# Kernel tuning notes

Hardware: AMD Instinct MI355X
Metric: run time of the kernel (lower is better)

Reference implementation:

```python
import jax, jax.numpy as jnp
import numpy as np

B, H, S, DH = 2, 16, 2048, 64

def setup_inputs() -> dict:
    key = jax.random.key(0)
    k1, k2, k3 = jax.random.split(key, 3)
    return {
        "query": jax.random.normal(k1, (B, H, S, DH), dtype=jnp.float32),
        "key": jax.random.normal(k2, (B, H, S, DH), dtype=jnp.float32),
        "value": jax.random.normal(k3, (B, H, S, DH), dtype=jnp.float32),
        "key_padding_mask": jnp.zeros((B, S), dtype=bool),
    }

def reference(query, key, value, key_padding_mask):
    # scores: [B, H, Sq, Sk]
    scale = 1.0 / jnp.sqrt(jnp.asarray(query.shape[-1], query.dtype))
    scores = jnp.einsum("bhqd,bhkd->bhqk", query, key) * scale
    # key padding mask broadcasts over heads and query positions
    scores = jnp.where(key_padding_mask[:, None, None, :], -jnp.inf, scores)
    attn = jax.nn.softmax(scores, axis=-1)
    # dropout is identity in eval mode (deterministic reference)
    out = jnp.einsum("bhqk,bhkd->bhqd", attn, value)
    # [B, H, S, Dh] -> [B, S, H*Dh]
    b, h, s, dh = out.shape
    return out.transpose(0, 2, 1, 3).reshape(b, s, h * dh)
```

## Files before the change

### kernel.cpp

```cpp
#include <hip/hip_runtime.h>

typedef __attribute__((ext_vector_type(4))) float f32x4;
typedef __attribute__((ext_vector_type(4))) short s16x4;
typedef __attribute__((ext_vector_type(8))) short s16x8;

constexpr int Bn = 2, Hn = 16, Sn = 2048, DHn = 64;
constexpr int TQ = 64;
constexpr int TK = 64;
constexpr int NT = Sn / TK;
constexpr int TILE_SH = TK * DHn;
constexpr float SHIFT = 16.0f;

__device__ __forceinline__ unsigned pk2(float a, float b) {
  unsigned ua = __builtin_bit_cast(unsigned, a);
  unsigned ub = __builtin_bit_cast(unsigned, b);
  ua += 0x7fffu + ((ua >> 16) & 1u);
  ub += 0x7fffu + ((ub >> 16) & 1u);
  return (ua >> 16) | (ub & 0xffff0000u);
}

__device__ __forceinline__ float fexp2(float x) {
#if __has_builtin(__builtin_amdgcn_exp2f)
  return __builtin_amdgcn_exp2f(x);
#else
  return exp2f(x);
#endif
}

__device__ __forceinline__ void gl2lds16(const short* g, short* l) {
  __builtin_amdgcn_global_load_lds(
      (const __attribute__((address_space(1))) void*)g,
      (__attribute__((address_space(3))) void*)l, 16, 0, 0);
}

__global__ __launch_bounds__(256, 4)
void prepack_kernel(const float* __restrict__ Kg, const float* __restrict__ Vg,
                    const unsigned char* __restrict__ maskg,
                    short* __restrict__ Kp, short* __restrict__ Vp,
                    float* __restrict__ biasg) {
  const int blk = blockIdx.x;
  const int tid = threadIdx.x;
  const float* Kt = Kg + (size_t)blk * TILE_SH;
  const float* Vt = Vg + (size_t)blk * TILE_SH;
  short* Kd = Kp + (size_t)blk * TILE_SH;
  short* Vd = Vp + (size_t)blk * TILE_SH;

  {
    const int r = tid >> 2;
    const int cb = (tid & 3) * 2;
#pragma unroll
    for (int cc = 0; cc < 2; ++cc) {
      int c = cb + cc;
      const float4* p = (const float4*)(Kt + (size_t)r * DHn + c * 8);
      float4 x = p[0], y = p[1];
      union { unsigned u[4]; s16x8 v; } tmp;
      tmp.u[0] = pk2(x.x, x.y); tmp.u[1] = pk2(x.z, x.w);
      tmp.u[2] = pk2(y.x, y.y); tmp.u[3] = pk2(y.z, y.w);
      *(s16x8*)&Kd[r * 64 + (c ^ (r & 7)) * 8] = tmp.v;
    }
  }
  {
    const int d = tid & 63;
    const int kb = (tid >> 6) * 16;
#pragma unroll
    for (int cc = 0; cc < 2; ++cc) {
      int k0 = kb + cc * 8;
      float v0[8];
#pragma unroll
      for (int j = 0; j < 8; ++j) v0[j] = Vt[(size_t)(k0 + j) * DHn + d];
      union { unsigned u[4]; s16x8 v; } tmp;
      tmp.u[0] = pk2(v0[0], v0[1]); tmp.u[1] = pk2(v0[2], v0[3]);
      tmp.u[2] = pk2(v0[4], v0[5]); tmp.u[3] = pk2(v0[6], v0[7]);
      int c = k0 >> 3;
      *(s16x8*)&Vd[d * 64 + (c ^ (d & 7)) * 8] = tmp.v;
    }
  }
  if (tid < TK) {
    const int bh = blk >> 5, t = blk & 31, b = bh >> 4;
    biasg[b * Sn + t * TK + tid] = maskg[b * Sn + t * TK + tid] ? -1e30f : -SHIFT;
  }
}

__global__ __launch_bounds__(128, 2)
void fattn_kernel(const float* __restrict__ Qg, const short* __restrict__ Kp,
                  const short* __restrict__ Vp, const float* __restrict__ biasg,
                  float* __restrict__ Og) {
  __shared__ __align__(16) short Ksh[2][TILE_SH];
  __shared__ __align__(16) short VTsh[2][TILE_SH];
  __shared__ __align__(16) short Psh[2 * 32 * 64];

  const int tid  = threadIdx.x;
  const int w    = tid >> 6;
  const int lane = tid & 63;
  const int n    = lane & 15;
  const int q4   = lane >> 4;
  const int swz  = n & 7;

  const int blk = blockIdx.x;
  const int bh  = blk & 31;
  const int qt  = blk >> 5;
  const int b   = bh >> 4;
  const int h   = bh & 15;

  const float* Qb = Qg + (size_t)bh * Sn * DHn;
  const short* Kt0 = Kp + (size_t)bh * NT * TILE_SH;
  const short* Vt0 = Vp + (size_t)bh * NT * TILE_SH;
  const float* bq0 = biasg + (size_t)b * Sn;

  const int q0 = qt * TQ + w * 32;

#pragma unroll
  for (int k = 0; k < 4; ++k) {
    gl2lds16(Kt0 + k * 1024 + tid * 8, &Ksh[0][k * 1024 + w * 512]);
    gl2lds16(Vt0 + k * 1024 + tid * 8, &VTsh[0][k * 1024 + w * 512]);
  }

  const float c1 = 0.125f * 1.4426950408889634f;
  s16x8 qf[2][2];
#pragma unroll
  for (int qg = 0; qg < 2; ++qg) {
    const float* qrow = Qb + (size_t)(q0 + qg * 16 + n) * DHn;
#pragma unroll
    for (int kc = 0; kc < 2; ++kc) {
      const float4* p = (const float4*)(qrow + kc * 32 + q4 * 8);
      float4 x = p[0], y = p[1];
      union { unsigned u[4]; s16x8 v; } tmp;
      tmp.u[0] = pk2(x.x * c1, x.y * c1);
      tmp.u[1] = pk2(x.z * c1, x.w * c1);
      tmp.u[2] = pk2(y.x * c1, y.y * c1);
      tmp.u[3] = pk2(y.z * c1, y.w * c1);
      qf[qg][kc] = tmp.v;
    }
  }

  const int c0    = q4 ^ swz;
  const int offA  = n * 64 + c0 * 8;
  const int offB  = n * 64 + (c0 ^ 4) * 8;
  const int prowA = (w * 32 + n) * 64;
  const int pc    = (q4 >> 1) ^ swz;
  const int pwo   = (q4 & 1) * 4;

  f32x4 Oa[2][4];
#pragma unroll
  for (int qg = 0; qg < 2; ++qg)
#pragma unroll
    for (int na = 0; na < 4; ++na) Oa[qg][na] = (f32x4){0.f, 0.f, 0.f, 0.f};
  float lsum[2] = {0.f, 0.f};

  for (int t = 0; t < NT; ++t) {
    const int cur = t & 1;
    __syncthreads();

    f32x4 bias[4];
    {
      const float* bq = bq0 + t * TK + q4 * 4;
#pragma unroll
      for (int mc = 0; mc < 4; ++mc) bias[mc] = *(const f32x4*)(bq + mc * 16);
    }
    asm volatile("" ::: "memory");

    if (t + 1 < NT) {
      const short* Ka = Kt0 + (t + 1) * TILE_SH;
      const short* Va = Vt0 + (t + 1) * TILE_SH;
#pragma unroll
      for (int k = 0; k < 4; ++k) {
        gl2lds16(Ka + k * 1024 + tid * 8, &Ksh[1 - cur][k * 1024 + w * 512]);
        gl2lds16(Va + k * 1024 + tid * 8, &VTsh[1 - cur][k * 1024 + w * 512]);
      }
    }

    s16x8 kf[4][2];
#pragma unroll
    for (int mc = 0; mc < 4; ++mc) {
      kf[mc][0] = *(const s16x8*)&Ksh[cur][mc * 1024 + offA];
      kf[mc][1] = *(const s16x8*)&Ksh[cur][mc * 1024 + offB];
    }

#pragma unroll
    for (int qg = 0; qg < 2; ++qg) {
      f32x4 sa[4];
#pragma unroll
      for (int mc = 0; mc < 4; ++mc) sa[mc] = bias[mc];
#pragma unroll
      for (int mc = 0; mc < 4; ++mc)
#pragma unroll
        for (int kc = 0; kc < 2; ++kc)
          sa[mc] = __builtin_amdgcn_mfma_f32_16x16x32_bf16(kf[mc][kc], qf[qg][kc], sa[mc], 0, 0, 0);

      const int prow = prowA + qg * (16 * 64);
      float ls = 0.f;
#pragma unroll
      for (int mc = 0; mc < 4; ++mc) {
        float p0 = fexp2(sa[mc][0]);
        float p1 = fexp2(sa[mc][1]);
        float p2 = fexp2(sa[mc][2]);
        float p3 = fexp2(sa[mc][3]);
        ls += (p0 + p1) + (p2 + p3);
        union { unsigned u[2]; s16x4 v4; } pw;
        pw.u[0] = pk2(p0, p1);
        pw.u[1] = pk2(p2, p3);
        *(s16x4*)&Psh[prow + ((pc ^ (2 * mc)) * 8) + pwo] = pw.v4;
      }
      ls += __shfl_xor(ls, 16);
      ls += __shfl_xor(ls, 32);
      lsum[qg] += ls;
    }

    s16x8 vf[4][2];
#pragma unroll
    for (int na = 0; na < 4; ++na) {
      vf[na][0] = *(const s16x8*)&VTsh[cur][na * 1024 + offA];
      vf[na][1] = *(const s16x8*)&VTsh[cur][na * 1024 + offB];
    }
#pragma unroll
    for (int qg = 0; qg < 2; ++qg) {
      const int prow = prowA + qg * (16 * 64);
      s16x8 pf[2];
      pf[0] = *(const s16x8*)&Psh[prow + ((q4 ^ swz) * 8)];
      pf[1] = *(const s16x8*)&Psh[prow + (((4 + q4) ^ swz) * 8)];
#pragma unroll
      for (int na = 0; na < 4; ++na)
#pragma unroll
        for (int kc = 0; kc < 2; ++kc)
          Oa[qg][na] = __builtin_amdgcn_mfma_f32_16x16x32_bf16(pf[kc], vf[na][kc], Oa[qg][na], 0, 0, 0);
    }
  }

#pragma unroll
  for (int qg = 0; qg < 2; ++qg) {
#pragma unroll
    for (int r = 0; r < 4; ++r) {
      float lr  = __shfl(lsum[qg], q4 * 4 + r);
      float inv = 1.0f / lr;
      int q = q0 + qg * 16 + q4 * 4 + r;
      float* orow = Og + (size_t)(b * Sn + q) * (Hn * DHn) + h * DHn;
#pragma unroll
      for (int na = 0; na < 4; ++na)
        orow[na * 16 + n] = Oa[qg][na][r] * inv;
    }
  }
}

extern "C" void kernel_launch(void* const* d_in, const int* in_sizes, int n_in,
                              void* d_out, int out_size, void* d_ws, size_t ws_size,
                              hipStream_t stream) {
  (void)in_sizes; (void)n_in; (void)ws_size; (void)out_size;
  const float* Q = (const float*)d_in[0];
  const float* K = (const float*)d_in[1];
  const float* V = (const float*)d_in[2];
  const unsigned char* mask = (const unsigned char*)d_in[3];
  float* out = (float*)d_out;

  short* Kp = (short*)d_ws;
  short* Vp = Kp + (size_t)Bn * Hn * Sn * DHn;
  float* biasg = (float*)(Vp + (size_t)Bn * Hn * Sn * DHn);

  hipLaunchKernelGGL(prepack_kernel, dim3(Bn * Hn * NT), dim3(256), 0, stream,
                     K, V, mask, Kp, Vp, biasg);
  hipLaunchKernelGGL(fattn_kernel, dim3(Bn * Hn * (Sn / TQ)), dim3(128), 0, stream,
                     Q, Kp, Vp, biasg, out);
}
```

Baseline: 157.5 us.

## Load K/V fragments straight to registers, compute row sums via MFMA

Drops the LDS double-buffering of K and V tiles and the per-iteration __syncthreads. Each wave now loads its MFMA fragments directly from global memory into registers, ping-ponging between two register sets so the next tile's loads overlap the current tile's compute. Softmax row sums are accumulated by an extra MFMA of the bf16 P fragments against a ones vector, replacing the shuffle reductions, and P packing uses the hardware bf16 convert when available. The cost is much higher register use and duplicated global/L2 traffic, since both waves fetch the same K/V tiles separately. The row sum is also now taken from bf16-rounded P instead of the fp32 values.

Measured after the change: 167.0 us. +6.0%, slower.

```diff
diff --git a/kernel.cpp b/kernel.cpp
--- a/kernel.cpp
+++ b/kernel.cpp
@@ -19,18 +19,23 @@
   return (ua >> 16) | (ub & 0xffff0000u);
 }
 
+__device__ __forceinline__ unsigned pkP(float a, float b) {
+#if __has_builtin(__builtin_amdgcn_cvt_pk_bf16_f32)
+  auto r = __builtin_amdgcn_cvt_pk_bf16_f32(a, b);
+  unsigned u;
+  __builtin_memcpy(&u, &r, 4);
+  return u;
+#else
+  return pk2(a, b);
+#endif
+}
+
 __device__ __forceinline__ float fexp2(float x) {
 #if __has_builtin(__builtin_amdgcn_exp2f)
   return __builtin_amdgcn_exp2f(x);
 #else
   return exp2f(x);
 #endif
-}
-
-__device__ __forceinline__ void gl2lds16(const short* g, short* l) {
-  __builtin_amdgcn_global_load_lds(
-      (const __attribute__((address_space(1))) void*)g,
-      (__attribute__((address_space(3))) void*)l, 16, 0, 0);
 }
 
 __global__ __launch_bounds__(256, 4)
@@ -85,8 +90,6 @@
 void fattn_kernel(const float* __restrict__ Qg, const short* __restrict__ Kp,
                   const short* __restrict__ Vp, const float* __restrict__ biasg,
                   float* __restrict__ Og) {
-  __shared__ __align__(16) short Ksh[2][TILE_SH];
-  __shared__ __align__(16) short VTsh[2][TILE_SH];
   __shared__ __align__(16) short Psh[2 * 32 * 64];
 
   const int tid  = threadIdx.x;
@@ -102,18 +105,12 @@
   const int b   = bh >> 4;
   const int h   = bh & 15;
 
-  const float* Qb = Qg + (size_t)bh * Sn * DHn;
+  const float* Qb  = Qg + (size_t)bh * Sn * DHn;
   const short* Kt0 = Kp + (size_t)bh * NT * TILE_SH;
   const short* Vt0 = Vp + (size_t)bh * NT * TILE_SH;
   const float* bq0 = biasg + (size_t)b * Sn;
 
   const int q0 = qt * TQ + w * 32;
-
-#pragma unroll
-  for (int k = 0; k < 4; ++k) {
-    gl2lds16(Kt0 + k * 1024 + tid * 8, &Ksh[0][k * 1024 + w * 512]);
-    gl2lds16(Vt0 + k * 1024 + tid * 8, &VTsh[0][k * 1024 + w * 512]);
-  }
 
   const float c1 = 0.125f * 1.4426950408889634f;
   s16x8 qf[2][2];
@@ -140,42 +137,36 @@
   const int pc    = (q4 >> 1) ^ swz;
   const int pwo   = (q4 & 1) * 4;
 
+  s16x8 ones;
+#pragma unroll
+  for (int i = 0; i < 8; ++i) ones[i] = (short)0x3F80;
+
   f32x4 Oa[2][4];
 #pragma unroll
   for (int qg = 0; qg < 2; ++qg)
 #pragma unroll
     for (int na = 0; na < 4; ++na) Oa[qg][na] = (f32x4){0.f, 0.f, 0.f, 0.f};
-  float lsum[2] = {0.f, 0.f};
-
-  for (int t = 0; t < NT; ++t) {
-    const int cur = t & 1;
-    __syncthreads();
-
+  f32x4 lacc[2] = {(f32x4){0.f, 0.f, 0.f, 0.f}, (f32x4){0.f, 0.f, 0.f, 0.f}};
+
+  auto load_tile = [&](s16x8 kf[4][2], s16x8 vf[4][2], int t) {
+    const short* Ka = Kt0 + (size_t)t * TILE_SH;
+    const short* Va = Vt0 + (size_t)t * TILE_SH;
+#pragma unroll
+    for (int mc = 0; mc < 4; ++mc) {
+      kf[mc][0] = *(const s16x8*)&Ka[mc * 1024 + offA];
+      kf[mc][1] = *(const s16x8*)&Ka[mc * 1024 + offB];
+      vf[mc][0] = *(const s16x8*)&Va[mc * 1024 + offA];
+      vf[mc][1] = *(const s16x8*)&Va[mc * 1024 + offB];
+    }
+  };
+
+  auto compute_tile = [&](s16x8 kf[4][2], s16x8 vf[4][2], int t) {
     f32x4 bias[4];
     {
       const float* bq = bq0 + t * TK + q4 * 4;
 #pragma unroll
       for (int mc = 0; mc < 4; ++mc) bias[mc] = *(const f32x4*)(bq + mc * 16);
     }
-    asm volatile("" ::: "memory");
-
-    if (t + 1 < NT) {
-      const short* Ka = Kt0 + (t + 1) * TILE_SH;
-      const short* Va = Vt0 + (t + 1) * TILE_SH;
-#pragma unroll
-      for (int k = 0; k < 4; ++k) {
-        gl2lds16(Ka + k * 1024 + tid * 8, &Ksh[1 - cur][k * 1024 + w * 512]);
-        gl2lds16(Va + k * 1024 + tid * 8, &VTsh[1 - cur][k * 1024 + w * 512]);
-      }
-    }
-
-    s16x8 kf[4][2];
-#pragma unroll
-    for (int mc = 0; mc < 4; ++mc) {
-      kf[mc][0] = *(const s16x8*)&Ksh[cur][mc * 1024 + offA];
-      kf[mc][1] = *(const s16x8*)&Ksh[cur][mc * 1024 + offB];
-    }
-
 #pragma unroll
     for (int qg = 0; qg < 2; ++qg) {
       f32x4 sa[4];
@@ -188,29 +179,17 @@
           sa[mc] = __builtin_amdgcn_mfma_f32_16x16x32_bf16(kf[mc][kc], qf[qg][kc], sa[mc], 0, 0, 0);
 
       const int prow = prowA + qg * (16 * 64);
-      float ls = 0.f;
 #pragma unroll
       for (int mc = 0; mc < 4; ++mc) {
         float p0 = fexp2(sa[mc][0]);
         float p1 = fexp2(sa[mc][1]);
         float p2 = fexp2(sa[mc][2]);
         float p3 = fexp2(sa[mc][3]);
-        ls += (p0 + p1) + (p2 + p3);
         union { unsigned u[2]; s16x4 v4; } pw;
-        pw.u[0] = pk2(p0, p1);
-        pw.u[1] = pk2(p2, p3);
+        pw.u[0] = pkP(p0, p1);
+        pw.u[1] = pkP(p2, p3);
         *(s16x4*)&Psh[prow + ((pc ^ (2 * mc)) * 8) + pwo] = pw.v4;
       }
-      ls += __shfl_xor(ls, 16);
-      ls += __shfl_xor(ls, 32);
-      lsum[qg] += ls;
-    }
-
-    s16x8 vf[4][2];
-#pragma unroll
-    for (int na = 0; na < 4; ++na) {
-      vf[na][0] = *(const s16x8*)&VTsh[cur][na * 1024 + offA];
-      vf[na][1] = *(const s16x8*)&VTsh[cur][na * 1024 + offB];
     }
 #pragma unroll
     for (int qg = 0; qg < 2; ++qg) {
@@ -218,20 +197,30 @@
       s16x8 pf[2];
       pf[0] = *(const s16x8*)&Psh[prow + ((q4 ^ swz) * 8)];
       pf[1] = *(const s16x8*)&Psh[prow + (((4 + q4) ^ swz) * 8)];
+      lacc[qg] = __builtin_amdgcn_mfma_f32_16x16x32_bf16(pf[0], ones, lacc[qg], 0, 0, 0);
+      lacc[qg] = __builtin_amdgcn_mfma_f32_16x16x32_bf16(pf[1], ones, lacc[qg], 0, 0, 0);
 #pragma unroll
       for (int na = 0; na < 4; ++na)
 #pragma unroll
         for (int kc = 0; kc < 2; ++kc)
           Oa[qg][na] = __builtin_amdgcn_mfma_f32_16x16x32_bf16(pf[kc], vf[na][kc], Oa[qg][na], 0, 0, 0);
     }
+  };
+
+  s16x8 kfA[4][2], vfA[4][2], kfB[4][2], vfB[4][2];
+  load_tile(kfA, vfA, 0);
+  for (int t = 0; t < NT; t += 2) {
+    if (t + 1 < NT) load_tile(kfB, vfB, t + 1);
+    compute_tile(kfA, vfA, t);
+    if (t + 2 < NT) load_tile(kfA, vfA, t + 2);
+    if (t + 1 < NT) compute_tile(kfB, vfB, t + 1);
   }
 
 #pragma unroll
   for (int qg = 0; qg < 2; ++qg) {
 #pragma unroll
     for (int r = 0; r < 4; ++r) {
-      float lr  = __shfl(lsum[qg], q4 * 4 + r);
-      float inv = 1.0f / lr;
+      float inv = 1.0f / lacc[qg][r];
       int q = q0 + qg * 16 + q4 * 4 + r;
       float* orow = Og + (size_t)(b * Sn + q) * (Hn * DHn) + h * DHn;
 #pragma unroll
```
